# Performance work log

Hardware: AMD Instinct MI355X
Metric: run time of the kernel (lower is better)

Reference implementation:

```python
import jax, jax.numpy as jnp
import numpy as np

NSITES = 100000
NYEARS = 20
NVIS = 2
HDIM = 64


def setup_inputs() -> dict:
    key = jax.random.key(0)
    ks = jax.random.split(key, 10)
    def w(k, shape, fan_in):
        return (jax.random.normal(k, shape, jnp.float32) / np.sqrt(fan_in)).astype(jnp.float32)
    return {
        "sxy0": jax.random.normal(ks[0], (1, NSITES, 1), jnp.float32),
        "sxy": jax.random.normal(ks[1], (NSITES, NYEARS - 1, 1), jnp.float32),
        "oxy": jax.random.normal(ks[2], (NSITES, NYEARS, NVIS), jnp.float32),
        # to_h0: Linear(1 -> 64)
        "W_h0": w(ks[3], (HDIM, 1), 1), "b_h0": jnp.zeros((HDIM,), jnp.float32),
        # to_h1: Linear(64 -> 64)
        "W_h1": w(ks[4], (HDIM, HDIM), HDIM), "b_h1": jnp.zeros((HDIM,), jnp.float32),
        # to_hrnn: RNN(input=1, hidden=64, relu)
        "W_ih": w(ks[5], (HDIM, 1), 1), "b_ih": jnp.zeros((HDIM,), jnp.float32),
        "W_hh": w(ks[6], (HDIM, HDIM), HDIM), "b_hh": jnp.zeros((HDIM,), jnp.float32),
        # to_psi0 / to_psi: Linear(64 -> 1)
        "W_psi0": w(ks[7], (1, HDIM), HDIM), "b_psi0": jnp.zeros((1,), jnp.float32),
        "W_psi": w(ks[8], (1, HDIM), HDIM), "b_psi": jnp.zeros((1,), jnp.float32),
        # to_p: Linear(65 -> 1)
        "W_p": w(ks[9], (1, HDIM + 1), HDIM + 1), "b_p": jnp.zeros((1,), jnp.float32),
    }


def reference(sxy0, sxy, oxy, W_h0, b_h0, W_h1, b_h1, W_ih, b_ih, W_hh, b_hh,
              W_psi0, b_psi0, W_psi, b_psi, W_p, b_p):
    # site embeddings -> initial hidden state
    hs = jax.nn.elu(sxy0 @ W_h0.T + b_h0)            # [1, N, H]
    h0 = jax.nn.elu(hs @ W_h1.T + b_h1)              # [1, N, H]

    # single-layer relu RNN, batch_first: sxy [N, T, 1], h0 [1, N, H]
    xs = jnp.swapaxes(sxy, 0, 1)                     # [T, N, 1]
    def step(h, x):
        h_new = jax.nn.relu(x @ W_ih.T + b_ih + h @ W_hh.T + b_hh)
        return h_new, h_new
    _, h_seq = jax.lax.scan(step, h0[0], xs)         # [T, N, H]
    h_out = jnp.swapaxes(h_seq, 0, 1)                # [N, T, H]

    psi0_out = jax.nn.sigmoid(h0 @ W_psi0.T + b_psi0)   # [1, N, 1]
    psi_out = jax.nn.sigmoid(h_out @ W_psi.T + b_psi)   # [N, T, 1]

    # detection prob p[i, t, j] = sigmoid(to_p(cat(H[i, t], oxy[i, t, j])))
    # where H[:, 0] = h0 and H[:, t] = h_out[:, t-1] for t >= 1
    H = jnp.concatenate([h0[0][:, None, :], h_out], axis=1)  # [N, Y, H]
    logits = H @ W_p[:, :HDIM].T + oxy * W_p[0, HDIM] + b_p  # [N, Y, NVIS]
    p = jax.nn.sigmoid(logits)
    return psi0_out, psi_out, p
```

## Files before the change

kernel.cpp:

```cpp
#include <hip/hip_runtime.h>
#include <math.h>

#define NSITES 100000
#define NYEARS 20
#define HDIM 64

typedef __bf16 bf16x8 __attribute__((ext_vector_type(8)));
typedef float f32x4 __attribute__((ext_vector_type(4)));

__device__ __forceinline__ float sigmoidf_(float x) { return 1.0f / (1.0f + __expf(-x)); }
__device__ __forceinline__ float eluf_(float x) { return x > 0.0f ? x : expm1f(x); }

__device__ __forceinline__ unsigned pack2_(float a, float b) {
    union { __bf16 h; unsigned short u; } x, y;
    x.h = (__bf16)a; y.h = (__bf16)b;
    return ((unsigned)y.u << 16) | (unsigned)x.u;
}

__device__ __forceinline__ bf16x8 cvt8_(const float* p) {
    float4 a = ((const float4*)p)[0];
    float4 b = ((const float4*)p)[1];
    bf16x8 r;
    r[0] = (__bf16)a.x; r[1] = (__bf16)a.y; r[2] = (__bf16)a.z; r[3] = (__bf16)a.w;
    r[4] = (__bf16)b.x; r[5] = (__bf16)b.y; r[6] = (__bf16)b.z; r[7] = (__bf16)b.w;
    return r;
}

__device__ __forceinline__ bf16x8 read_bfrag_(const unsigned short* hp) {
    union { bf16x8 v; uint2 u[2]; } r;
    r.u[0] = *(const uint2*)(hp);
    r.u[1] = *(const uint2*)(hp + 4);
    return r.v;
}

__global__ __launch_bounds__(64, 2)
void rnet_kernel(const float* __restrict__ sxy0,
                 const float* __restrict__ sxy,
                 const float* __restrict__ oxy,
                 const float* __restrict__ W_h0, const float* __restrict__ b_h0,
                 const float* __restrict__ W_h1, const float* __restrict__ b_h1,
                 const float* __restrict__ W_ih, const float* __restrict__ b_ih,
                 const float* __restrict__ W_hh, const float* __restrict__ b_hh,
                 const float* __restrict__ W_psi0, const float* __restrict__ b_psi0,
                 const float* __restrict__ W_psi, const float* __restrict__ b_psi,
                 const float* __restrict__ W_p, const float* __restrict__ b_p,
                 float* __restrict__ out)
{
    const int lane = threadIdx.x;
    const int s = lane & 15;
    const int q = lane >> 4;
    const int base = blockIdx.x * 16;
    const int site = base + s;

    __shared__ __align__(16) unsigned short h_sh[16 * 68];
    __shared__ __align__(16) float psi_sh[16 * 19];
    __shared__ __align__(16) float p_sh[16 * 40];

    float* __restrict__ out_psi0 = out;
    float* __restrict__ out_psi  = out + NSITES;
    float* __restrict__ out_p    = out + 20 * NSITES;

    {
        const float s0v = sxy0[site];
        bf16x8 bf0[2];
#pragma unroll
        for (int kt = 0; kt < 2; ++kt) {
            const float* wp = W_h0 + kt * 32 + q * 8;
            const float* bp = b_h0 + kt * 32 + q * 8;
            float4 w0 = ((const float4*)wp)[0], w1 = ((const float4*)wp)[1];
            float4 c0 = ((const float4*)bp)[0], c1 = ((const float4*)bp)[1];
            float v[8];
            v[0] = eluf_(fmaf(s0v, w0.x, c0.x)); v[1] = eluf_(fmaf(s0v, w0.y, c0.y));
            v[2] = eluf_(fmaf(s0v, w0.z, c0.z)); v[3] = eluf_(fmaf(s0v, w0.w, c0.w));
            v[4] = eluf_(fmaf(s0v, w1.x, c1.x)); v[5] = eluf_(fmaf(s0v, w1.y, c1.y));
            v[6] = eluf_(fmaf(s0v, w1.z, c1.z)); v[7] = eluf_(fmaf(s0v, w1.w, c1.w));
#pragma unroll
            for (int j = 0; j < 8; ++j) bf0[kt][j] = (__bf16)v[j];
        }

        f32x4 acc[4];
#pragma unroll
        for (int mt = 0; mt < 4; ++mt) {
            float4 b1 = *(const float4*)(b_h1 + mt * 16 + q * 4);
            acc[mt][0] = b1.x; acc[mt][1] = b1.y; acc[mt][2] = b1.z; acc[mt][3] = b1.w;
        }
#pragma unroll
        for (int kt = 0; kt < 2; ++kt)
#pragma unroll
            for (int mt = 0; mt < 4; ++mt) {
                bf16x8 a = cvt8_(W_h1 + (mt * 16 + s) * 64 + kt * 32 + q * 8);
                acc[mt] = __builtin_amdgcn_mfma_f32_16x16x32_bf16(a, bf0[kt], acc[mt], 0, 0, 0);
            }
#pragma unroll
        for (int mt = 0; mt < 4; ++mt) {
            float v0 = eluf_(acc[mt][0]), v1 = eluf_(acc[mt][1]);
            float v2 = eluf_(acc[mt][2]), v3 = eluf_(acc[mt][3]);
            uint2 pk; pk.x = pack2_(v0, v1); pk.y = pack2_(v2, v3);
            *(uint2*)&h_sh[s * 68 + mt * 16 + q * 4] = pk;
        }
    }

    bf16x8 a_hh[4][2], a_head[2];
#pragma unroll
    for (int mt = 0; mt < 4; ++mt)
#pragma unroll
        for (int kt = 0; kt < 2; ++kt)
            a_hh[mt][kt] = cvt8_(W_hh + (mt * 16 + s) * 64 + kt * 32 + q * 8);
    {
        const float* hrow = (s == 1) ? W_p : ((s == 2) ? W_psi0 : W_psi);
#pragma unroll
        for (int kt = 0; kt < 2; ++kt) a_head[kt] = cvt8_(hrow + kt * 32 + q * 8);
    }

    f32x4 biasD[4], wihD[4];
#pragma unroll
    for (int mt = 0; mt < 4; ++mt) {
        const int r0 = mt * 16 + q * 4;
        float4 bi = *(const float4*)(b_ih + r0);
        float4 bh = *(const float4*)(b_hh + r0);
        float4 wi = *(const float4*)(W_ih + r0);
        biasD[mt][0] = bi.x + bh.x; biasD[mt][1] = bi.y + bh.y;
        biasD[mt][2] = bi.z + bh.z; biasD[mt][3] = bi.w + bh.w;
        wihD[mt][0] = wi.x; wihD[mt][1] = wi.y; wihD[mt][2] = wi.z; wihD[mt][3] = wi.w;
    }
    f32x4 headC;
    headC[0] = (q == 0) ? b_psi[0]  : 0.0f;
    headC[1] = (q == 0) ? b_p[0]    : 0.0f;
    headC[2] = (q == 0) ? b_psi0[0] : 0.0f;
    headC[3] = 0.0f;
    const float wpo = W_p[HDIM];

    const float* sxy_l = sxy + (size_t)site * (NYEARS - 1);
    const float* oxy_l = oxy + (size_t)site * (NYEARS * 2);

    for (int t = 1; t < NYEARS; ++t) {
        bf16x8 bf[2];
        bf[0] = read_bfrag_(&h_sh[s * 68 + 0  + q * 8]);
        bf[1] = read_bfrag_(&h_sh[s * 68 + 32 + q * 8]);

        f32x4 acc[4], accH = headC;
#pragma unroll
        for (int mt = 0; mt < 4; ++mt) acc[mt] = biasD[mt];
#pragma unroll
        for (int kt = 0; kt < 2; ++kt) {
#pragma unroll
            for (int mt = 0; mt < 4; ++mt)
                acc[mt] = __builtin_amdgcn_mfma_f32_16x16x32_bf16(a_hh[mt][kt], bf[kt], acc[mt], 0, 0, 0);
            accH = __builtin_amdgcn_mfma_f32_16x16x32_bf16(a_head[kt], bf[kt], accH, 0, 0, 0);
        }

        const float x = sxy_l[t - 1];
#pragma unroll
        for (int mt = 0; mt < 4; ++mt) {
            float v0 = fmaxf(fmaf(x, wihD[mt][0], acc[mt][0]), 0.0f);
            float v1 = fmaxf(fmaf(x, wihD[mt][1], acc[mt][1]), 0.0f);
            float v2 = fmaxf(fmaf(x, wihD[mt][2], acc[mt][2]), 0.0f);
            float v3 = fmaxf(fmaf(x, wihD[mt][3], acc[mt][3]), 0.0f);
            uint2 pk; pk.x = pack2_(v0, v1); pk.y = pack2_(v2, v3);
            *(uint2*)&h_sh[s * 68 + mt * 16 + q * 4] = pk;
        }

        if (q == 0) {
            float2 ox = *(const float2*)(oxy_l + (t - 1) * 2);
            float p0 = sigmoidf_(fmaf(wpo, ox.x, accH[1]));
            float p1 = sigmoidf_(fmaf(wpo, ox.y, accH[1]));
            float2 pp; pp.x = p0; pp.y = p1;
            *(float2*)&p_sh[s * 40 + (t - 1) * 2] = pp;
            if (t == 1) {
                out_psi0[site] = sigmoidf_(accH[2]);
            } else {
                psi_sh[s * 19 + (t - 2)] = sigmoidf_(accH[0]);
            }
        }
    }

    {
        bf16x8 bf[2];
        bf[0] = read_bfrag_(&h_sh[s * 68 + 0  + q * 8]);
        bf[1] = read_bfrag_(&h_sh[s * 68 + 32 + q * 8]);
        f32x4 accH = headC;
#pragma unroll
        for (int kt = 0; kt < 2; ++kt)
            accH = __builtin_amdgcn_mfma_f32_16x16x32_bf16(a_head[kt], bf[kt], accH, 0, 0, 0);
        if (q == 0) {
            float2 ox = *(const float2*)(oxy_l + 19 * 2);
            float p0 = sigmoidf_(fmaf(wpo, ox.x, accH[1]));
            float p1 = sigmoidf_(fmaf(wpo, ox.y, accH[1]));
            float2 pp; pp.x = p0; pp.y = p1;
            *(float2*)&p_sh[s * 40 + 38] = pp;
            psi_sh[s * 19 + 18] = sigmoidf_(accH[0]);
        }
    }

    __syncthreads();

#pragma unroll
    for (int r = 0; r < 5; ++r) {
        int i = r * 64 + lane;
        if (i < 16 * 19) out_psi[(size_t)base * 19 + i] = psi_sh[i];
    }
    f32x4* pg = (f32x4*)(out_p + (size_t)base * 40);
    const f32x4* ps = (const f32x4*)p_sh;
#pragma unroll
    for (int r = 0; r < 3; ++r) {
        int i = r * 64 + lane;
        if (i < 160) pg[i] = ps[i];
    }
}

extern "C" void kernel_launch(void* const* d_in, const int* in_sizes, int n_in,
                              void* d_out, int out_size, void* d_ws, size_t ws_size,
                              hipStream_t stream) {
    const float* sxy0   = (const float*)d_in[0];
    const float* sxy    = (const float*)d_in[1];
    const float* oxy    = (const float*)d_in[2];
    const float* W_h0   = (const float*)d_in[3];
    const float* b_h0   = (const float*)d_in[4];
    const float* W_h1   = (const float*)d_in[5];
    const float* b_h1   = (const float*)d_in[6];
    const float* W_ih   = (const float*)d_in[7];
    const float* b_ih   = (const float*)d_in[8];
    const float* W_hh   = (const float*)d_in[9];
    const float* b_hh   = (const float*)d_in[10];
    const float* W_psi0 = (const float*)d_in[11];
    const float* b_psi0 = (const float*)d_in[12];
    const float* W_psi  = (const float*)d_in[13];
    const float* b_psi  = (const float*)d_in[14];
    const float* W_p    = (const float*)d_in[15];
    const float* b_p    = (const float*)d_in[16];

    float* out = (float*)d_out;

    dim3 block(64);
    dim3 grid(NSITES / 16);
    rnet_kernel<<<grid, block, 0, stream>>>(
        sxy0, sxy, oxy, W_h0, b_h0, W_h1, b_h1, W_ih, b_ih, W_hh, b_hh,
        W_psi0, b_psi0, W_psi, b_psi, W_p, b_p, out);
}
```

Measured before the change: 167.6 us.

## Keep RNN hidden state in registers via permuted weight rows, defer sigmoids

Permutes the row order of the W_hh and W_h1 MFMA A-operands so each step's accumulator output lands directly in the B-fragment layout of the next step. This removes the per-timestep round trip of the hidden state through shared memory. It also preloads the sxy sequence into registers, fully unrolls the time loop, and stores raw logits. Sigmoids and the oxy term are then applied in a coalesced epilogue, so q==0 lanes no longer do scattered per-step work. The cost is higher register pressure from the unroll and the xs array.

```diff
diff --git a/kernel.cpp b/kernel.cpp
--- a/kernel.cpp
+++ b/kernel.cpp
@@ -10,12 +10,6 @@
 
 __device__ __forceinline__ float sigmoidf_(float x) { return 1.0f / (1.0f + __expf(-x)); }
 __device__ __forceinline__ float eluf_(float x) { return x > 0.0f ? x : expm1f(x); }
-
-__device__ __forceinline__ unsigned pack2_(float a, float b) {
-    union { __bf16 h; unsigned short u; } x, y;
-    x.h = (__bf16)a; y.h = (__bf16)b;
-    return ((unsigned)y.u << 16) | (unsigned)x.u;
-}
 
 __device__ __forceinline__ bf16x8 cvt8_(const float* p) {
     float4 a = ((const float4*)p)[0];
@@ -26,11 +20,11 @@
     return r;
 }
 
-__device__ __forceinline__ bf16x8 read_bfrag_(const unsigned short* hp) {
-    union { bf16x8 v; uint2 u[2]; } r;
-    r.u[0] = *(const uint2*)(hp);
-    r.u[1] = *(const uint2*)(hp + 4);
-    return r.v;
+__device__ __forceinline__ bf16x8 pack_bf_(f32x4 lo, f32x4 hi) {
+    bf16x8 r;
+    r[0] = (__bf16)lo[0]; r[1] = (__bf16)lo[1]; r[2] = (__bf16)lo[2]; r[3] = (__bf16)lo[3];
+    r[4] = (__bf16)hi[0]; r[5] = (__bf16)hi[1]; r[6] = (__bf16)hi[2]; r[7] = (__bf16)hi[3];
+    return r;
 }
 
 __global__ __launch_bounds__(64, 2)
@@ -49,17 +43,58 @@
     const int lane = threadIdx.x;
     const int s = lane & 15;
     const int q = lane >> 4;
+    const int sq = s >> 2, sr = s & 3;
     const int base = blockIdx.x * 16;
     const int site = base + s;
 
-    __shared__ __align__(16) unsigned short h_sh[16 * 68];
-    __shared__ __align__(16) float psi_sh[16 * 19];
-    __shared__ __align__(16) float p_sh[16 * 40];
+    __shared__ __align__(16) float pL_sh[16 * 20];
+    __shared__ __align__(16) float psiL_sh[16 * 19];
 
     float* __restrict__ out_psi0 = out;
     float* __restrict__ out_psi  = out + NSITES;
     float* __restrict__ out_p    = out + 20 * NSITES;
 
+    bf16x8 a_hh[4][2];
+#pragma unroll
+    for (int mt = 0; mt < 4; ++mt) {
+        const int ar = 32 * (mt >> 1) + 8 * sq + 4 * (mt & 1) + sr;
+#pragma unroll
+        for (int kt = 0; kt < 2; ++kt)
+            a_hh[mt][kt] = cvt8_(W_hh + ar * 64 + kt * 32 + q * 8);
+    }
+    bf16x8 a_head[2];
+    {
+        const float* hrow = (s == 1) ? W_p : ((s == 2) ? W_psi0 : W_psi);
+#pragma unroll
+        for (int kt = 0; kt < 2; ++kt) a_head[kt] = cvt8_(hrow + kt * 32 + q * 8);
+    }
+
+    f32x4 biasD[4], wihD[4];
+#pragma unroll
+    for (int mt = 0; mt < 4; ++mt) {
+        const int dr = 32 * (mt >> 1) + 8 * q + 4 * (mt & 1);
+        float4 bi = *(const float4*)(b_ih + dr);
+        float4 bh = *(const float4*)(b_hh + dr);
+        float4 wi = *(const float4*)(W_ih + dr);
+        biasD[mt][0] = bi.x + bh.x; biasD[mt][1] = bi.y + bh.y;
+        biasD[mt][2] = bi.z + bh.z; biasD[mt][3] = bi.w + bh.w;
+        wihD[mt][0] = wi.x; wihD[mt][1] = wi.y; wihD[mt][2] = wi.z; wihD[mt][3] = wi.w;
+    }
+    f32x4 headC;
+    headC[0] = (q == 0) ? b_psi[0]  : 0.0f;
+    headC[1] = (q == 0) ? b_p[0]    : 0.0f;
+    headC[2] = (q == 0) ? b_psi0[0] : 0.0f;
+    headC[3] = 0.0f;
+    const float wpo = W_p[HDIM];
+
+    float xs[NYEARS - 1];
+    {
+        const float* sxy_l = sxy + (size_t)site * (NYEARS - 1);
+#pragma unroll
+        for (int i = 0; i < NYEARS - 1; ++i) xs[i] = sxy_l[i];
+    }
+
+    bf16x8 bf[2];
     {
         const float s0v = sxy0[site];
         bf16x8 bf0[2];
@@ -81,63 +116,29 @@
         f32x4 acc[4];
 #pragma unroll
         for (int mt = 0; mt < 4; ++mt) {
-            float4 b1 = *(const float4*)(b_h1 + mt * 16 + q * 4);
+            const int dr = 32 * (mt >> 1) + 8 * q + 4 * (mt & 1);
+            float4 b1 = *(const float4*)(b_h1 + dr);
             acc[mt][0] = b1.x; acc[mt][1] = b1.y; acc[mt][2] = b1.z; acc[mt][3] = b1.w;
         }
 #pragma unroll
         for (int kt = 0; kt < 2; ++kt)
 #pragma unroll
             for (int mt = 0; mt < 4; ++mt) {
-                bf16x8 a = cvt8_(W_h1 + (mt * 16 + s) * 64 + kt * 32 + q * 8);
+                const int ar = 32 * (mt >> 1) + 8 * sq + 4 * (mt & 1) + sr;
+                bf16x8 a = cvt8_(W_h1 + ar * 64 + kt * 32 + q * 8);
                 acc[mt] = __builtin_amdgcn_mfma_f32_16x16x32_bf16(a, bf0[kt], acc[mt], 0, 0, 0);
             }
-#pragma unroll
-        for (int mt = 0; mt < 4; ++mt) {
-            float v0 = eluf_(acc[mt][0]), v1 = eluf_(acc[mt][1]);
-            float v2 = eluf_(acc[mt][2]), v3 = eluf_(acc[mt][3]);
-            uint2 pk; pk.x = pack2_(v0, v1); pk.y = pack2_(v2, v3);
-            *(uint2*)&h_sh[s * 68 + mt * 16 + q * 4] = pk;
-        }
-    }
-
-    bf16x8 a_hh[4][2], a_head[2];
-#pragma unroll
-    for (int mt = 0; mt < 4; ++mt)
-#pragma unroll
-        for (int kt = 0; kt < 2; ++kt)
-            a_hh[mt][kt] = cvt8_(W_hh + (mt * 16 + s) * 64 + kt * 32 + q * 8);
-    {
-        const float* hrow = (s == 1) ? W_p : ((s == 2) ? W_psi0 : W_psi);
-#pragma unroll
-        for (int kt = 0; kt < 2; ++kt) a_head[kt] = cvt8_(hrow + kt * 32 + q * 8);
-    }
-
-    f32x4 biasD[4], wihD[4];
-#pragma unroll
-    for (int mt = 0; mt < 4; ++mt) {
-        const int r0 = mt * 16 + q * 4;
-        float4 bi = *(const float4*)(b_ih + r0);
-        float4 bh = *(const float4*)(b_hh + r0);
-        float4 wi = *(const float4*)(W_ih + r0);
-        biasD[mt][0] = bi.x + bh.x; biasD[mt][1] = bi.y + bh.y;
-        biasD[mt][2] = bi.z + bh.z; biasD[mt][3] = bi.w + bh.w;
-        wihD[mt][0] = wi.x; wihD[mt][1] = wi.y; wihD[mt][2] = wi.z; wihD[mt][3] = wi.w;
-    }
-    f32x4 headC;
-    headC[0] = (q == 0) ? b_psi[0]  : 0.0f;
-    headC[1] = (q == 0) ? b_p[0]    : 0.0f;
-    headC[2] = (q == 0) ? b_psi0[0] : 0.0f;
-    headC[3] = 0.0f;
-    const float wpo = W_p[HDIM];
-
-    const float* sxy_l = sxy + (size_t)site * (NYEARS - 1);
-    const float* oxy_l = oxy + (size_t)site * (NYEARS * 2);
-
+        f32x4 e[4];
+#pragma unroll
+        for (int mt = 0; mt < 4; ++mt)
+#pragma unroll
+            for (int r = 0; r < 4; ++r) e[mt][r] = eluf_(acc[mt][r]);
+        bf[0] = pack_bf_(e[0], e[1]);
+        bf[1] = pack_bf_(e[2], e[3]);
+    }
+
+#pragma unroll
     for (int t = 1; t < NYEARS; ++t) {
-        bf16x8 bf[2];
-        bf[0] = read_bfrag_(&h_sh[s * 68 + 0  + q * 8]);
-        bf[1] = read_bfrag_(&h_sh[s * 68 + 32 + q * 8]);
-
         f32x4 acc[4], accH = headC;
 #pragma unroll
         for (int mt = 0; mt < 4; ++mt) acc[mt] = biasD[mt];
@@ -149,46 +150,34 @@
             accH = __builtin_amdgcn_mfma_f32_16x16x32_bf16(a_head[kt], bf[kt], accH, 0, 0, 0);
         }
 
-        const float x = sxy_l[t - 1];
-#pragma unroll
-        for (int mt = 0; mt < 4; ++mt) {
-            float v0 = fmaxf(fmaf(x, wihD[mt][0], acc[mt][0]), 0.0f);
-            float v1 = fmaxf(fmaf(x, wihD[mt][1], acc[mt][1]), 0.0f);
-            float v2 = fmaxf(fmaf(x, wihD[mt][2], acc[mt][2]), 0.0f);
-            float v3 = fmaxf(fmaf(x, wihD[mt][3], acc[mt][3]), 0.0f);
-            uint2 pk; pk.x = pack2_(v0, v1); pk.y = pack2_(v2, v3);
-            *(uint2*)&h_sh[s * 68 + mt * 16 + q * 4] = pk;
-        }
+        const float x = xs[t - 1];
+        f32x4 hn[4];
+#pragma unroll
+        for (int mt = 0; mt < 4; ++mt)
+#pragma unroll
+            for (int r = 0; r < 4; ++r)
+                hn[mt][r] = fmaxf(fmaf(x, wihD[mt][r], acc[mt][r]), 0.0f);
+        bf[0] = pack_bf_(hn[0], hn[1]);
+        bf[1] = pack_bf_(hn[2], hn[3]);
 
         if (q == 0) {
-            float2 ox = *(const float2*)(oxy_l + (t - 1) * 2);
-            float p0 = sigmoidf_(fmaf(wpo, ox.x, accH[1]));
-            float p1 = sigmoidf_(fmaf(wpo, ox.y, accH[1]));
-            float2 pp; pp.x = p0; pp.y = p1;
-            *(float2*)&p_sh[s * 40 + (t - 1) * 2] = pp;
+            pL_sh[s * 20 + (t - 1)] = accH[1];
             if (t == 1) {
                 out_psi0[site] = sigmoidf_(accH[2]);
             } else {
-                psi_sh[s * 19 + (t - 2)] = sigmoidf_(accH[0]);
+                psiL_sh[s * 19 + (t - 2)] = accH[0];
             }
         }
     }
 
     {
-        bf16x8 bf[2];
-        bf[0] = read_bfrag_(&h_sh[s * 68 + 0  + q * 8]);
-        bf[1] = read_bfrag_(&h_sh[s * 68 + 32 + q * 8]);
         f32x4 accH = headC;
 #pragma unroll
         for (int kt = 0; kt < 2; ++kt)
             accH = __builtin_amdgcn_mfma_f32_16x16x32_bf16(a_head[kt], bf[kt], accH, 0, 0, 0);
         if (q == 0) {
-            float2 ox = *(const float2*)(oxy_l + 19 * 2);
-            float p0 = sigmoidf_(fmaf(wpo, ox.x, accH[1]));
-            float p1 = sigmoidf_(fmaf(wpo, ox.y, accH[1]));
-            float2 pp; pp.x = p0; pp.y = p1;
-            *(float2*)&p_sh[s * 40 + 38] = pp;
-            psi_sh[s * 19 + 18] = sigmoidf_(accH[0]);
+            pL_sh[s * 20 + 19] = accH[1];
+            psiL_sh[s * 19 + 18] = accH[0];
         }
     }
 
@@ -197,14 +186,16 @@
 #pragma unroll
     for (int r = 0; r < 5; ++r) {
         int i = r * 64 + lane;
-        if (i < 16 * 19) out_psi[(size_t)base * 19 + i] = psi_sh[i];
-    }
-    f32x4* pg = (f32x4*)(out_p + (size_t)base * 40);
-    const f32x4* ps = (const f32x4*)p_sh;
-#pragma unroll
-    for (int r = 0; r < 3; ++r) {
+        if (i < 16 * 19)
+            out_psi[(size_t)base * 19 + i] = sigmoidf_(psiL_sh[i]);
+    }
+    const float* oxy_b = oxy + (size_t)base * 40;
+    float* outp_b = out_p + (size_t)base * 40;
+#pragma unroll
+    for (int r = 0; r < 10; ++r) {
         int i = r * 64 + lane;
-        if (i < 160) pg[i] = ps[i];
+        float lg = pL_sh[i >> 1];
+        outp_b[i] = sigmoidf_(fmaf(wpo, oxy_b[i], lg));
     }
 }
 
```

Result: faster. 152.7 us (-8.9%).
